# Optimization experiments

Measured on AMD Instinct MI355X. Metric: run time of the kernel, lower is better.

Reference implementation:

```python
import jax, jax.numpy as jnp
import numpy as np

B, C, T = 128, 16, 16384
WINDOW_RATIO = 0.25
W = int(np.ceil(WINDOW_RATIO * T))  # warp_size = 4096
LMAX = T + W                        # max warped length (scale=2 case)
SCALES = (0.5, 2.0)


def setup_inputs() -> dict:
    key = jax.random.key(0)
    k1, k2, k3 = jax.random.split(key, 3)
    x = jax.random.normal(k1, (B, C, T), dtype=jnp.float32)
    # np.random.randint(low=1, high=T - W - 1)
    window_starts = jax.random.randint(k2, (B,), 1, T - W - 1).astype(jnp.int32)
    # per-sample scale choice from {0.5, 2.0}; new_len = int(W * scale)
    pick = jax.random.bernoulli(k3, 0.5, (B,))
    new_len = jnp.where(pick, int(W * SCALES[1]), int(W * SCALES[0])).astype(jnp.int32)
    return {"x": x, "window_starts": window_starts, "new_len": new_len}


def _warp_sample(xc, s, nl):
    """Window-warp one sample. xc: (C, T); s, nl: scalar int32.

    Stage 1 builds the (padded) 'warped' signal of true length L = T + nl - W:
      [0, s)        -> original samples
      [s, s+nl)     -> window resampled from W to nl points (np.interp)
      [s+nl, L)     -> original tail samples
    Every warped[j] is a linear interp of xc at a fractional source position,
    so we compute positions then gather+lerp (exactly np.interp with xp=arange).
    Stage 2 resamples warped (length L) back to T points (second np.interp).
    """
    j = jnp.arange(LMAX, dtype=jnp.float32)
    sf = s.astype(jnp.float32)
    nlf = nl.astype(jnp.float32)
    in_win = (j >= sf) & (j < sf + nlf)
    after = j >= sf + nlf
    # source position in the original time axis for each warped index j
    pos = jnp.where(
        in_win,
        sf + (j - sf) * (W - 1.0) / jnp.maximum(nlf - 1.0, 1.0),
        jnp.where(after, j - nlf + W, j),
    )
    pos = jnp.clip(pos, 0.0, T - 1.0)
    lo = jnp.floor(pos).astype(jnp.int32)
    hi = jnp.minimum(lo + 1, T - 1)
    f = pos - lo
    warped = xc[:, lo] * (1.0 - f) + xc[:, hi] * f  # (C, LMAX); entries past L unused

    L_i = T + nl - W  # true warped length (traced int)
    Lf = L_i.astype(jnp.float32)
    # np.interp(arange(T), linspace(0, T-1, L), warped): query index = t*(L-1)/(T-1)
    q = jnp.arange(T, dtype=jnp.float32) * (Lf - 1.0) / (T - 1.0)
    qlo = jnp.floor(q).astype(jnp.int32)
    qhi = jnp.minimum(qlo + 1, L_i - 1)
    qf = q - qlo
    return warped[:, qlo] * (1.0 - qf) + warped[:, qhi] * qf  # (C, T)


def reference(x, window_starts, new_len):
    # x: (B, C, T) -> module transposes to (B, T, C), warps per sample/channel,
    # transposes back; equivalent to operating on (C, T) directly per sample.
    return jax.vmap(_warp_sample)(x, window_starts, new_len)
```

## Files before the change

### kernel.cpp

```cpp
#include <hip/hip_runtime.h>

#define NB 128
#define NC 16
#define NT 16384
#define NW 4096

__global__ __launch_bounds__(256) void rww_kernel(
    const float* __restrict__ x,
    const int* __restrict__ window_starts,
    const int* __restrict__ new_len,
    float* __restrict__ out)
{
    const int b = blockIdx.y;
    const int t = blockIdx.x * 256 + threadIdx.x;

    const int s  = window_starts[b];
    const int nl = new_len[b];
    const float sf  = (float)s;
    const float nlf = (float)nl;
    const float den = fmaxf(nlf - 1.0f, 1.0f);
    const int   L   = NT + nl - NW;
    const float Lf  = (float)L;

    float qpos = (float)t * (Lf - 1.0f) / (float)(NT - 1);
    int   qlo  = (int)floorf(qpos);
    int   qhi  = min(qlo + 1, L - 1);
    float qf   = qpos - (float)qlo;

    int lo0, hi0, lo1, hi1;
    float f0, f1;
    {
        float jf = (float)qlo;
        float pos;
        if (jf >= sf + nlf)      pos = jf - nlf + (float)NW;
        else if (jf >= sf)       pos = sf + (jf - sf) * (float)(NW - 1) / den;
        else                     pos = jf;
        pos = fminf(fmaxf(pos, 0.0f), (float)(NT - 1));
        lo0 = (int)floorf(pos);
        hi0 = min(lo0 + 1, NT - 1);
        f0  = pos - (float)lo0;
    }
    {
        float jf = (float)qhi;
        float pos;
        if (jf >= sf + nlf)      pos = jf - nlf + (float)NW;
        else if (jf >= sf)       pos = sf + (jf - sf) * (float)(NW - 1) / den;
        else                     pos = jf;
        pos = fminf(fmaxf(pos, 0.0f), (float)(NT - 1));
        lo1 = (int)floorf(pos);
        hi1 = min(lo1 + 1, NT - 1);
        f1  = pos - (float)lo1;
    }

    const float* xb = x   + (size_t)b * NC * NT;
    float*       ob = out + (size_t)b * NC * NT;

    const float g0 = 1.0f - f0;
    const float g1 = 1.0f - f1;
    const float gq = 1.0f - qf;

    #pragma unroll
    for (int c = 0; c < NC; ++c) {
        const float* xc = xb + c * NT;
        float a0 = xc[lo0];
        float b0 = xc[hi0];
        float a1 = xc[lo1];
        float b1 = xc[hi1];
        float v0 = a0 * g0 + b0 * f0;
        float v1 = a1 * g1 + b1 * f1;
        ob[c * NT + t] = v0 * gq + v1 * qf;
    }
}

extern "C" void kernel_launch(void* const* d_in, const int* in_sizes, int n_in,
                              void* d_out, int out_size, void* d_ws, size_t ws_size,
                              hipStream_t stream) {
    const float* x  = (const float*)d_in[0];
    const int*   ws = (const int*)d_in[1];
    const int*   nl = (const int*)d_in[2];
    float*       out = (float*)d_out;

    dim3 grid(NT / 256, NB);
    dim3 block(256);
    rww_kernel<<<grid, block, 0, stream>>>(x, ws, nl, out);
}
```

Baseline: 51.26 us.

## Process four outputs per thread using vectorized window loads and dense weights

Each thread now produces four consecutive output samples. It loads an aligned 16-float window of each channel with float4 loads, then applies a precomputed 4x16 weight matrix that folds both interpolation stages into one. Results are written with a vectorized nontemporal store. This replaces eight scattered scalar gathers per output with coalesced vector loads, but adds 1024 FMAs per channel group and a large register footprint. It also relies on the four outputs' source span fitting in 16 samples, which holds for the scales used here.

Measured after the change: 48.51 us. -5.4%, faster.

```diff
diff --git a/kernel.cpp b/kernel.cpp
--- a/kernel.cpp
+++ b/kernel.cpp
@@ -5,14 +5,16 @@
 #define NT 16384
 #define NW 4096
 
+typedef float f32x4 __attribute__((ext_vector_type(4)));
+
 __global__ __launch_bounds__(256) void rww_kernel(
     const float* __restrict__ x,
     const int* __restrict__ window_starts,
     const int* __restrict__ new_len,
     float* __restrict__ out)
 {
-    const int b = blockIdx.y;
-    const int t = blockIdx.x * 256 + threadIdx.x;
+    const int b  = blockIdx.y;
+    const int t0 = (blockIdx.x * 256 + threadIdx.x) * 4;
 
     const int s  = window_starts[b];
     const int nl = new_len[b];
@@ -22,65 +24,95 @@
     const int   L   = NT + nl - NW;
     const float Lf  = (float)L;
 
-    float qpos = (float)t * (Lf - 1.0f) / (float)(NT - 1);
-    int   qlo  = (int)floorf(qpos);
-    int   qhi  = min(qlo + 1, L - 1);
-    float qf   = qpos - (float)qlo;
+    int   lo0[4], hi0[4], lo1[4], hi1[4];
+    float f0[4], f1[4], qf[4];
 
-    int lo0, hi0, lo1, hi1;
-    float f0, f1;
-    {
-        float jf = (float)qlo;
-        float pos;
-        if (jf >= sf + nlf)      pos = jf - nlf + (float)NW;
-        else if (jf >= sf)       pos = sf + (jf - sf) * (float)(NW - 1) / den;
-        else                     pos = jf;
-        pos = fminf(fmaxf(pos, 0.0f), (float)(NT - 1));
-        lo0 = (int)floorf(pos);
-        hi0 = min(lo0 + 1, NT - 1);
-        f0  = pos - (float)lo0;
+    #pragma unroll
+    for (int i = 0; i < 4; ++i) {
+        const int t = t0 + i;
+        float qpos = (float)t * (Lf - 1.0f) / (float)(NT - 1);
+        int   ql   = (int)floorf(qpos);
+        int   qh   = min(ql + 1, L - 1);
+        qf[i]      = qpos - (float)ql;
+
+        {
+            float jf = (float)ql;
+            float pos;
+            if (jf >= sf + nlf)      pos = jf - nlf + (float)NW;
+            else if (jf >= sf)       pos = sf + (jf - sf) * (float)(NW - 1) / den;
+            else                     pos = jf;
+            pos = fminf(fmaxf(pos, 0.0f), (float)(NT - 1));
+            lo0[i] = (int)floorf(pos);
+            hi0[i] = min(lo0[i] + 1, NT - 1);
+            f0[i]  = pos - (float)lo0[i];
+        }
+        {
+            float jf = (float)qh;
+            float pos;
+            if (jf >= sf + nlf)      pos = jf - nlf + (float)NW;
+            else if (jf >= sf)       pos = sf + (jf - sf) * (float)(NW - 1) / den;
+            else                     pos = jf;
+            pos = fminf(fmaxf(pos, 0.0f), (float)(NT - 1));
+            lo1[i] = (int)floorf(pos);
+            hi1[i] = min(lo1[i] + 1, NT - 1);
+            f1[i]  = pos - (float)lo1[i];
+        }
     }
-    {
-        float jf = (float)qhi;
-        float pos;
-        if (jf >= sf + nlf)      pos = jf - nlf + (float)NW;
-        else if (jf >= sf)       pos = sf + (jf - sf) * (float)(NW - 1) / den;
-        else                     pos = jf;
-        pos = fminf(fmaxf(pos, 0.0f), (float)(NT - 1));
-        lo1 = (int)floorf(pos);
-        hi1 = min(lo1 + 1, NT - 1);
-        f1  = pos - (float)lo1;
+
+    int base = lo0[0] & ~3;
+    base = min(base, NT - 16);
+
+    float w[4][16];
+    #pragma unroll
+    for (int i = 0; i < 4; ++i) {
+        const float g0 = 1.0f - f0[i];
+        const float g1 = 1.0f - f1[i];
+        const float gq = 1.0f - qf[i];
+        #pragma unroll
+        for (int k = 0; k < 16; ++k) {
+            const int kk = base + k;
+            float w0 = (kk == lo0[i] ? g0 : 0.0f) + (kk == hi0[i] ? f0[i] : 0.0f);
+            float w1 = (kk == lo1[i] ? g1 : 0.0f) + (kk == hi1[i] ? f1[i] : 0.0f);
+            w[i][k] = gq * w0 + qf[i] * w1;
+        }
     }
 
     const float* xb = x   + (size_t)b * NC * NT;
     float*       ob = out + (size_t)b * NC * NT;
 
-    const float g0 = 1.0f - f0;
-    const float g1 = 1.0f - f1;
-    const float gq = 1.0f - qf;
-
-    #pragma unroll
+    #pragma unroll 4
     for (int c = 0; c < NC; ++c) {
-        const float* xc = xb + c * NT;
-        float a0 = xc[lo0];
-        float b0 = xc[hi0];
-        float a1 = xc[lo1];
-        float b1 = xc[hi1];
-        float v0 = a0 * g0 + b0 * f0;
-        float v1 = a1 * g1 + b1 * f1;
-        ob[c * NT + t] = v0 * gq + v1 * qf;
+        const float* xc = xb + c * NT + base;
+        const f32x4 v0 = *(const f32x4*)(xc);
+        const f32x4 v1 = *(const f32x4*)(xc + 4);
+        const f32x4 v2 = *(const f32x4*)(xc + 8);
+        const f32x4 v3 = *(const f32x4*)(xc + 12);
+        const float win[16] = {v0.x, v0.y, v0.z, v0.w,
+                               v1.x, v1.y, v1.z, v1.w,
+                               v2.x, v2.y, v2.z, v2.w,
+                               v3.x, v3.y, v3.z, v3.w};
+        f32x4 r;
+        #pragma unroll
+        for (int i = 0; i < 4; ++i) {
+            float acc = 0.0f;
+            #pragma unroll
+            for (int k = 0; k < 16; ++k)
+                acc += w[i][k] * win[k];
+            r[i] = acc;
+        }
+        __builtin_nontemporal_store(r, (f32x4*)(ob + c * NT + t0));
     }
 }
 
 extern "C" void kernel_launch(void* const* d_in, const int* in_sizes, int n_in,
                               void* d_out, int out_size, void* d_ws, size_t ws_size,
                               hipStream_t stream) {
-    const float* x  = (const float*)d_in[0];
-    const int*   ws = (const int*)d_in[1];
-    const int*   nl = (const int*)d_in[2];
+    const float* x   = (const float*)d_in[0];
+    const int*   ws  = (const int*)d_in[1];
+    const int*   nl  = (const int*)d_in[2];
     float*       out = (float*)d_out;
 
-    dim3 grid(NT / 256, NB);
+    dim3 grid(NT / (256 * 4), NB);
     dim3 block(256);
     rww_kernel<<<grid, block, 0, stream>>>(x, ws, nl, out);
 }
```

## Stage per-block source window into LDS and use nontemporal output stores

Applied to the files above, without the earlier changes.

Each block computes the start of the source range its 256 outputs touch and cooperatively loads a 480-sample span for all 16 channels into shared memory with 16-byte vector loads. The four gathers per channel then read from LDS instead of global memory. Output stores are marked nontemporal to avoid polluting the cache. The fixed span assumes the source footprint of 256 outputs stays within 480 samples (max slope about 2x when the warp compresses), which could go out of bounds if that assumption fails.

Result: slower. 63.45 us (+23.8%).

```diff
diff --git a/kernel.cpp b/kernel.cpp
--- a/kernel.cpp
+++ b/kernel.cpp
@@ -4,6 +4,10 @@
 #define NC 16
 #define NT 16384
 #define NW 4096
+#define TPB 256
+#define SPAN 480
+
+typedef float f32x4 __attribute__((ext_vector_type(4)));
 
 __global__ __launch_bounds__(256) void rww_kernel(
     const float* __restrict__ x,
@@ -11,8 +15,11 @@
     const int* __restrict__ new_len,
     float* __restrict__ out)
 {
-    const int b = blockIdx.y;
-    const int t = blockIdx.x * 256 + threadIdx.x;
+    __shared__ float lds[NC][SPAN];
+
+    const int b  = blockIdx.y;
+    const int t0 = blockIdx.x * TPB;
+    const int t  = t0 + threadIdx.x;
 
     const int s  = window_starts[b];
     const int nl = new_len[b];
@@ -22,12 +29,40 @@
     const int   L   = NT + nl - NW;
     const float Lf  = (float)L;
 
+    int winstart;
+    {
+        float qpos = (float)t0 * (Lf - 1.0f) / (float)(NT - 1);
+        int   ql   = (int)floorf(qpos);
+        float jf   = (float)ql;
+        float pos;
+        if (jf >= sf + nlf)      pos = jf - nlf + (float)NW;
+        else if (jf >= sf)       pos = sf + (jf - sf) * (float)(NW - 1) / den;
+        else                     pos = jf;
+        pos = fminf(fmaxf(pos, 0.0f), (float)(NT - 1));
+        winstart = ((int)floorf(pos)) & ~3;
+        winstart = min(winstart, NT - SPAN);
+        if (winstart < 0) winstart = 0;
+    }
+
+    const float* xb = x + (size_t)b * NC * NT;
+    #pragma unroll
+    for (int it = 0; it < (NC * SPAN / 4 + TPB - 1) / TPB; ++it) {
+        int idx = it * TPB + threadIdx.x;
+        if (idx < NC * (SPAN / 4)) {
+            int c   = idx / (SPAN / 4);
+            int col = (idx % (SPAN / 4)) * 4;
+            f32x4 v = *(const f32x4*)(xb + c * NT + winstart + col);
+            *(f32x4*)&lds[c][col] = v;
+        }
+    }
+    __syncthreads();
+
     float qpos = (float)t * (Lf - 1.0f) / (float)(NT - 1);
     int   qlo  = (int)floorf(qpos);
     int   qhi  = min(qlo + 1, L - 1);
     float qf   = qpos - (float)qlo;
 
-    int lo0, hi0, lo1, hi1;
+    int r0lo, r0hi, r1lo, r1hi;
     float f0, f1;
     {
         float jf = (float)qlo;
@@ -36,9 +71,11 @@
         else if (jf >= sf)       pos = sf + (jf - sf) * (float)(NW - 1) / den;
         else                     pos = jf;
         pos = fminf(fmaxf(pos, 0.0f), (float)(NT - 1));
-        lo0 = (int)floorf(pos);
-        hi0 = min(lo0 + 1, NT - 1);
-        f0  = pos - (float)lo0;
+        int lo = (int)floorf(pos);
+        int hi = min(lo + 1, NT - 1);
+        f0   = pos - (float)lo;
+        r0lo = lo - winstart;
+        r0hi = hi - winstart;
     }
     {
         float jf = (float)qhi;
@@ -47,40 +84,40 @@
         else if (jf >= sf)       pos = sf + (jf - sf) * (float)(NW - 1) / den;
         else                     pos = jf;
         pos = fminf(fmaxf(pos, 0.0f), (float)(NT - 1));
-        lo1 = (int)floorf(pos);
-        hi1 = min(lo1 + 1, NT - 1);
-        f1  = pos - (float)lo1;
+        int lo = (int)floorf(pos);
+        int hi = min(lo + 1, NT - 1);
+        f1   = pos - (float)lo;
+        r1lo = lo - winstart;
+        r1hi = hi - winstart;
     }
-
-    const float* xb = x   + (size_t)b * NC * NT;
-    float*       ob = out + (size_t)b * NC * NT;
 
     const float g0 = 1.0f - f0;
     const float g1 = 1.0f - f1;
     const float gq = 1.0f - qf;
 
+    float* ob = out + (size_t)b * NC * NT + t;
+
     #pragma unroll
     for (int c = 0; c < NC; ++c) {
-        const float* xc = xb + c * NT;
-        float a0 = xc[lo0];
-        float b0 = xc[hi0];
-        float a1 = xc[lo1];
-        float b1 = xc[hi1];
+        float a0 = lds[c][r0lo];
+        float b0 = lds[c][r0hi];
+        float a1 = lds[c][r1lo];
+        float b1 = lds[c][r1hi];
         float v0 = a0 * g0 + b0 * f0;
         float v1 = a1 * g1 + b1 * f1;
-        ob[c * NT + t] = v0 * gq + v1 * qf;
+        __builtin_nontemporal_store(v0 * gq + v1 * qf, ob + c * NT);
     }
 }
 
 extern "C" void kernel_launch(void* const* d_in, const int* in_sizes, int n_in,
                               void* d_out, int out_size, void* d_ws, size_t ws_size,
                               hipStream_t stream) {
-    const float* x  = (const float*)d_in[0];
-    const int*   ws = (const int*)d_in[1];
-    const int*   nl = (const int*)d_in[2];
+    const float* x   = (const float*)d_in[0];
+    const int*   ws  = (const int*)d_in[1];
+    const int*   nl  = (const int*)d_in[2];
     float*       out = (float*)d_out;
 
-    dim3 grid(NT / 256, NB);
-    dim3 block(256);
+    dim3 grid(NT / TPB, NB);
+    dim3 block(TPB);
     rww_kernel<<<grid, block, 0, stream>>>(x, ws, nl, out);
 }
```
